# Performance work log

Hardware: AMD Instinct MI355X
Metric: run time of the kernel (lower is better)

Reference implementation:

```python
import jax, jax.numpy as jnp
import numpy as np

C0 = 32   # number of 0e (scalar) channels
C1 = 16   # number of 1o (vector) channels
NG = 1024 # num_graphs
N = 300000
F = C0 * (C0 + 1) // 2 + C1 * (C1 + 1) // 2  # 664 invariant outputs of TensorSquare->0e


def setup_inputs() -> dict:
    key = jax.random.key(0)
    k1, k2, k3 = jax.random.split(key, 3)
    node_ft = jax.random.normal(k1, (N, C0 + 3 * C1), dtype=jnp.float32)
    batch_index = jnp.sort(jax.random.randint(k2, (N,), 0, NG, dtype=jnp.int32))
    # o3.Linear-style init: normal / sqrt(fan_in)
    W = jax.random.normal(k3, (F, 1), dtype=jnp.float32) / np.float32(np.sqrt(F))
    return {"node_ft": node_ft, "batch_index": batch_index, "num_graphs": NG, "W": W}


def tensor_square_0e(node_ft):
    # Equivariant tensor square keeping only 0e (invariant) outputs:
    #  - symmetric products of scalar channels s_i * s_j (i<=j)
    #  - dot products of vector channels v_i . v_j (i<=j), component-normalized
    s = node_ft[:, :C0]                      # [N, C0]
    v = node_ft[:, C0:].reshape(-1, C1, 3)   # [N, C1, 3]
    i0, j0 = jnp.triu_indices(C0)
    i1, j1 = jnp.triu_indices(C1)
    ts_s = s[:, i0] * s[:, j0]                                  # [N, 528]
    vdot = jnp.einsum('nic,njc->nij', v, v) / jnp.float32(np.sqrt(3.0))
    ts_v = vdot[:, i1, j1]                                      # [N, 136]
    return jnp.concatenate([ts_s, ts_v], axis=1)                # [N, 664]


def reference(node_ft, batch_index, num_graphs, W):
    x = tensor_square_0e(node_ft)            # [N, F]
    x = jax.nn.selu(x)
    x = x @ W                                # [N, 1] attention logits (1x0e)
    ex = jnp.exp(x)                          # [N, 1]
    z = jax.ops.segment_sum(ex, batch_index, num_segments=num_graphs)  # [G, 1]
    attn = ex / z[batch_index]               # segment softmax weights [N, 1]
    out = jax.ops.segment_sum(node_ft * attn, batch_index, num_segments=num_graphs)
    return out                               # [G, C0 + 3*C1]
```

## Files before the change

kernel.cpp:

```cpp
#include <hip/hip_runtime.h>


typedef float f2 __attribute__((ext_vector_type(2)));

#define C0 32
#define C1 16
#define NODE_F 80
#define NG_CONST 1024
#define NPB 320

#define SELU_SCALE 1.0507009873554804934193349852946
#define SELU_ALPHA 1.6732632423543772848170429916717
#define LOG2E      1.4426950408889634073599246810019

#define CS_SCALE 1.2011224087864498f
#define CV_SCALE 0.91271231102878545f

#define WS_S 0
#define WS_Z 81920
#define WS_W 82944

__device__ __forceinline__ int ks_idx(int i, int j) { return i * C0 - (i * (i - 1)) / 2 + (j - i); }
__device__ __forceinline__ int kv_idx(int i, int j) { return 528 + i * C1 - (i * (i - 1)) / 2 + (j - i); }

__global__ __launch_bounds__(256) void prep_kernel(
    const float* __restrict__ W, float* __restrict__ ws)
{
    const int t = blockIdx.x * blockDim.x + threadIdx.x;
    if (t < 82944) {
        ws[t] = 0.0f;
    } else {
        int u = t - 82944;
        if (u < 512) {
            int i = u >> 4, q = u & 15;
            int j0 = 2 * q, j1 = 2 * q + 1;
            ws[WS_W + 2 * u]     = (j0 >= i) ? W[ks_idx(i, j0)] : 0.0f;
            ws[WS_W + 2 * u + 1] = (j1 >= i) ? W[ks_idx(i, j1)] : 0.0f;
        } else if (u < 640) {
            int v = u - 512;
            int i = v >> 3, q = v & 7;
            int j0 = 2 * q, j1 = 2 * q + 1;
            ws[WS_W + 1024 + 2 * v]     = (j0 >= i) ? W[kv_idx(i, j0)] : 0.0f;
            ws[WS_W + 1024 + 2 * v + 1] = (j1 >= i) ? W[kv_idx(i, j1)] : 0.0f;
        }
    }
}

__global__ __launch_bounds__(NPB, 2) void main_kernel(
    const float* __restrict__ nf, const int* __restrict__ bi,
    const float* __restrict__ ws, float* __restrict__ S,
    float* __restrict__ z, int N)
{
    __shared__ __align__(16) float Wlds[1280];
    __shared__ float exl[NPB];
    __shared__ int   bil[NPB];

    const int tid  = threadIdx.x;
    const int base = blockIdx.x * NPB;
    const float4* g4 = (const float4*)nf;

    #pragma unroll
    for (int u = tid; u < 1280; u += NPB) Wlds[u] = ws[WS_W + u];

    const int  n     = base + tid;
    const bool valid = (n < N);
    const int  nn    = valid ? n : (N - 1);
    bil[tid] = bi[nn];
    __syncthreads();

    float4 row4[20];
    #pragma unroll
    for (int q = 0; q < 20; ++q) row4[q] = g4[(size_t)nn * 20 + q];
    const float* row = (const float*)row4;

    const f2* WsL = (const f2*)Wlds;
    const f2* WvL = (const f2*)(Wlds + 1024);

    f2 accA[2], accB[2];
    accA[0] = (f2)0.f; accA[1] = (f2)0.f; accB[0] = (f2)0.f; accB[1] = (f2)0.f;

    {
        f2 s2[C0 / 2];
        #pragma unroll
        for (int q = 0; q < C0 / 2; ++q)
            s2[q] = f2{row[2 * q], row[2 * q + 1]} * CS_SCALE;
        #pragma unroll
        for (int i = 0; i < C0; ++i) {
            const float si = (i & 1) ? s2[i >> 1].y : s2[i >> 1].x;
            const f2 si2 = f2{si, si};
            #pragma unroll
            for (int q = i >> 1; q < C0 / 2; ++q) {
                f2 f = si2 * s2[q];
                f2 p = __builtin_elementwise_max(f, (f2)0.f);
                f2 m = __builtin_elementwise_min(f, (f2)0.f);
                f2 e; e.x = __builtin_amdgcn_exp2f(m.x);
                      e.y = __builtin_amdgcn_exp2f(m.y);
                f2 w = WsL[i * 16 + q];
                accA[q & 1] = __builtin_elementwise_fma(w, p, accA[q & 1]);
                accB[q & 1] = __builtin_elementwise_fma(w, e, accB[q & 1]);
            }
        }
    }
    {
        f2 vp[C1 / 2][3];
        #pragma unroll
        for (int q = 0; q < C1 / 2; ++q) {
            #pragma unroll
            for (int c = 0; c < 3; ++c)
                vp[q][c] = f2{row[C0 + 6 * q + c], row[C0 + 6 * q + 3 + c]} * CV_SCALE;
        }
        #pragma unroll
        for (int i = 0; i < C1; ++i) {
            const int iq = i >> 1;
            const float vi0 = (i & 1) ? vp[iq][0].y : vp[iq][0].x;
            const float vi1 = (i & 1) ? vp[iq][1].y : vp[iq][1].x;
            const float vi2 = (i & 1) ? vp[iq][2].y : vp[iq][2].x;
            #pragma unroll
            for (int q = i >> 1; q < C1 / 2; ++q) {
                f2 f = vp[q][0] * f2{vi0, vi0};
                f = __builtin_elementwise_fma(vp[q][1], f2{vi1, vi1}, f);
                f = __builtin_elementwise_fma(vp[q][2], f2{vi2, vi2}, f);
                f2 p = __builtin_elementwise_max(f, (f2)0.f);
                f2 m = __builtin_elementwise_min(f, (f2)0.f);
                f2 e; e.x = __builtin_amdgcn_exp2f(m.x);
                      e.y = __builtin_amdgcn_exp2f(m.y);
                f2 w = WvL[i * 8 + q];
                accA[q & 1] = __builtin_elementwise_fma(w, p, accA[q & 1]);
                accB[q & 1] = __builtin_elementwise_fma(w, e, accB[q & 1]);
            }
        }
    }

    const float A1 = accA[0].x + accA[0].y + accA[1].x + accA[1].y;
    const float A2 = accB[0].x + accB[0].y + accB[1].x + accB[1].y;
    const float l2 = fmaf((float)SELU_SCALE, A1,
                          (float)(SELU_SCALE * SELU_ALPHA * LOG2E) * A2);
    exl[tid] = valid ? __builtin_amdgcn_exp2f(l2) : 0.0f;
    __syncthreads();

    const int no = tid / 20;
    const int c4 = tid % 20;
    int cg = bil[no * 20];
    float4 acc = make_float4(0.f, 0.f, 0.f, 0.f);
    float  zacc = 0.0f;

    #pragma unroll
    for (int k = 0; k < 20; ++k) {
        const int nl = no * 20 + k;
        const int g2 = bil[nl];
        if (g2 != cg) {
            unsafeAtomicAdd(&S[cg * NODE_F + c4 * 4 + 0], acc.x);
            unsafeAtomicAdd(&S[cg * NODE_F + c4 * 4 + 1], acc.y);
            unsafeAtomicAdd(&S[cg * NODE_F + c4 * 4 + 2], acc.z);
            unsafeAtomicAdd(&S[cg * NODE_F + c4 * 4 + 3], acc.w);
            if (c4 == 0) unsafeAtomicAdd(&z[cg], zacc);
            acc = make_float4(0.f, 0.f, 0.f, 0.f); zacc = 0.0f; cg = g2;
        }
        int idx = base + nl; if (idx > N - 1) idx = N - 1;
        const float  w = exl[nl];
        const float4 v = g4[(size_t)idx * 20 + c4];
        acc.x = fmaf(v.x, w, acc.x); acc.y = fmaf(v.y, w, acc.y);
        acc.z = fmaf(v.z, w, acc.z); acc.w = fmaf(v.w, w, acc.w);
        zacc += w;
    }
    unsafeAtomicAdd(&S[cg * NODE_F + c4 * 4 + 0], acc.x);
    unsafeAtomicAdd(&S[cg * NODE_F + c4 * 4 + 1], acc.y);
    unsafeAtomicAdd(&S[cg * NODE_F + c4 * 4 + 2], acc.z);
    unsafeAtomicAdd(&S[cg * NODE_F + c4 * 4 + 3], acc.w);
    if (c4 == 0) unsafeAtomicAdd(&z[cg], zacc);
}

__global__ __launch_bounds__(256) void divide_kernel(
    const float* __restrict__ S, const float* __restrict__ z,
    float* __restrict__ out)
{
    const int t = blockIdx.x * blockDim.x + threadIdx.x;
    if (t >= NG_CONST * NODE_F) return;
    const float zz = z[t / NODE_F];
    out[t] = (zz > 0.0f) ? (S[t] / zz) : 0.0f;
}

extern "C" void kernel_launch(void* const* d_in, const int* in_sizes, int n_in,
                              void* d_out, int out_size, void* d_ws, size_t ws_size,
                              hipStream_t stream) {
    const float* nf = (const float*)d_in[0];
    const int*   bi = (const int*)d_in[1];
    const float* W  = (const float*)d_in[3];
    float* out = (float*)d_out;

    const int N = in_sizes[0] / NODE_F;
    float* ws = (float*)d_ws;
    float* S  = ws + WS_S;
    float* z  = ws + WS_Z;

    hipLaunchKernelGGL(prep_kernel, dim3(332), dim3(256), 0, stream, W, ws);
    hipLaunchKernelGGL(main_kernel, dim3((N + NPB - 1) / NPB), dim3(NPB), 0, stream,
                       nf, bi, ws, S, z, N);
    hipLaunchKernelGGL(divide_kernel, dim3((NG_CONST * NODE_F + 255) / 256), dim3(256),
                       0, stream, S, z, out);
}
```

Measured before the change: 194.5 us.

## Split each node's tensor-square work across two threads with shuffle reduction

After: 253.3 us. 1.3x slower.

```diff
diff --git a/kernel.cpp b/kernel.cpp
--- a/kernel.cpp
+++ b/kernel.cpp
@@ -7,7 +7,8 @@
 #define C1 16
 #define NODE_F 80
 #define NG_CONST 1024
-#define NPB 320
+#define NPB 160
+#define TPB 320
 
 #define SELU_SCALE 1.0507009873554804934193349852946
 #define SELU_ALPHA 1.6732632423543772848170429916717
@@ -46,7 +47,7 @@
     }
 }
 
-__global__ __launch_bounds__(NPB, 2) void main_kernel(
+__global__ __launch_bounds__(TPB, 8) void main_kernel(
     const float* __restrict__ nf, const int* __restrict__ bi,
     const float* __restrict__ ws, float* __restrict__ S,
     float* __restrict__ z, int N)
@@ -60,12 +61,18 @@
     const float4* g4 = (const float4*)nf;
 
     #pragma unroll
-    for (int u = tid; u < 1280; u += NPB) Wlds[u] = ws[WS_W + u];
-
-    const int  n     = base + tid;
+    for (int u = tid; u < 1280; u += TPB) Wlds[u] = ws[WS_W + u];
+
+    if (tid < NPB) {
+        int idx = base + tid;
+        bil[tid] = bi[idx > N - 1 ? N - 1 : idx];
+    }
+
+    const int  ln    = tid >> 1;
+    const int  p     = tid & 1;
+    const int  n     = base + ln;
     const bool valid = (n < N);
     const int  nn    = valid ? n : (N - 1);
-    bil[tid] = bi[nn];
     __syncthreads();
 
     float4 row4[20];
@@ -85,18 +92,19 @@
         for (int q = 0; q < C0 / 2; ++q)
             s2[q] = f2{row[2 * q], row[2 * q + 1]} * CS_SCALE;
         #pragma unroll
-        for (int i = 0; i < C0; ++i) {
-            const float si = (i & 1) ? s2[i >> 1].y : s2[i >> 1].x;
+        for (int k = 0; k < C0 / 2; ++k) {
+            const int i = 2 * k + p;
+            const float si = p ? s2[k].y : s2[k].x;
             const f2 si2 = f2{si, si};
             #pragma unroll
-            for (int q = i >> 1; q < C0 / 2; ++q) {
+            for (int q = k; q < C0 / 2; ++q) {
                 f2 f = si2 * s2[q];
-                f2 p = __builtin_elementwise_max(f, (f2)0.f);
-                f2 m = __builtin_elementwise_min(f, (f2)0.f);
+                f2 pp = __builtin_elementwise_max(f, (f2)0.f);
+                f2 m  = __builtin_elementwise_min(f, (f2)0.f);
                 f2 e; e.x = __builtin_amdgcn_exp2f(m.x);
                       e.y = __builtin_amdgcn_exp2f(m.y);
                 f2 w = WsL[i * 16 + q];
-                accA[q & 1] = __builtin_elementwise_fma(w, p, accA[q & 1]);
+                accA[q & 1] = __builtin_elementwise_fma(w, pp, accA[q & 1]);
                 accB[q & 1] = __builtin_elementwise_fma(w, e, accB[q & 1]);
             }
         }
@@ -110,43 +118,46 @@
                 vp[q][c] = f2{row[C0 + 6 * q + c], row[C0 + 6 * q + 3 + c]} * CV_SCALE;
         }
         #pragma unroll
-        for (int i = 0; i < C1; ++i) {
-            const int iq = i >> 1;
-            const float vi0 = (i & 1) ? vp[iq][0].y : vp[iq][0].x;
-            const float vi1 = (i & 1) ? vp[iq][1].y : vp[iq][1].x;
-            const float vi2 = (i & 1) ? vp[iq][2].y : vp[iq][2].x;
+        for (int k = 0; k < C1 / 2; ++k) {
+            const int i = 2 * k + p;
+            const float vi0 = p ? vp[k][0].y : vp[k][0].x;
+            const float vi1 = p ? vp[k][1].y : vp[k][1].x;
+            const float vi2 = p ? vp[k][2].y : vp[k][2].x;
             #pragma unroll
-            for (int q = i >> 1; q < C1 / 2; ++q) {
+            for (int q = k; q < C1 / 2; ++q) {
                 f2 f = vp[q][0] * f2{vi0, vi0};
                 f = __builtin_elementwise_fma(vp[q][1], f2{vi1, vi1}, f);
                 f = __builtin_elementwise_fma(vp[q][2], f2{vi2, vi2}, f);
-                f2 p = __builtin_elementwise_max(f, (f2)0.f);
-                f2 m = __builtin_elementwise_min(f, (f2)0.f);
+                f2 pp = __builtin_elementwise_max(f, (f2)0.f);
+                f2 m  = __builtin_elementwise_min(f, (f2)0.f);
                 f2 e; e.x = __builtin_amdgcn_exp2f(m.x);
                       e.y = __builtin_amdgcn_exp2f(m.y);
                 f2 w = WvL[i * 8 + q];
-                accA[q & 1] = __builtin_elementwise_fma(w, p, accA[q & 1]);
+                accA[q & 1] = __builtin_elementwise_fma(w, pp, accA[q & 1]);
                 accB[q & 1] = __builtin_elementwise_fma(w, e, accB[q & 1]);
             }
         }
     }
 
-    const float A1 = accA[0].x + accA[0].y + accA[1].x + accA[1].y;
-    const float A2 = accB[0].x + accB[0].y + accB[1].x + accB[1].y;
+    float A1 = accA[0].x + accA[0].y + accA[1].x + accA[1].y;
+    float A2 = accB[0].x + accB[0].y + accB[1].x + accB[1].y;
+    A1 += __shfl_xor(A1, 1);
+    A2 += __shfl_xor(A2, 1);
     const float l2 = fmaf((float)SELU_SCALE, A1,
                           (float)(SELU_SCALE * SELU_ALPHA * LOG2E) * A2);
-    exl[tid] = valid ? __builtin_amdgcn_exp2f(l2) : 0.0f;
+    if (p == 0) exl[ln] = valid ? __builtin_amdgcn_exp2f(l2) : 0.0f;
     __syncthreads();
 
     const int no = tid / 20;
     const int c4 = tid % 20;
-    int cg = bil[no * 20];
+    const int nb = no * 10;
+    int cg = bil[nb];
     float4 acc = make_float4(0.f, 0.f, 0.f, 0.f);
     float  zacc = 0.0f;
 
     #pragma unroll
-    for (int k = 0; k < 20; ++k) {
-        const int nl = no * 20 + k;
+    for (int k = 0; k < 10; ++k) {
+        const int nl = nb + k;
         const int g2 = bil[nl];
         if (g2 != cg) {
             unsafeAtomicAdd(&S[cg * NODE_F + c4 * 4 + 0], acc.x);
@@ -194,7 +205,7 @@
     float* z  = ws + WS_Z;
 
     hipLaunchKernelGGL(prep_kernel, dim3(332), dim3(256), 0, stream, W, ws);
-    hipLaunchKernelGGL(main_kernel, dim3((N + NPB - 1) / NPB), dim3(NPB), 0, stream,
+    hipLaunchKernelGGL(main_kernel, dim3((N + NPB - 1) / NPB), dim3(TPB), 0, stream,
                        nf, bi, ws, S, z, N);
     hipLaunchKernelGGL(divide_kernel, dim3((NG_CONST * NODE_F + 255) / 256), dim3(256),
                        0, stream, S, z, out);
```
